# Kernel optimization log

Hardware: AMD Instinct MI355X
Metric: run time of the kernel (lower is better)

## Reference

```python
import jax, jax.numpy as jnp
import numpy as np

FD = 8  # flow_downsample


def equal_conv(x, w, b):
    # StyleGAN EqualConv2d: weight scaled by 1/sqrt(fan_in) at runtime, 3x3, pad 1
    scale = 1.0 / np.sqrt(w.shape[1] * w.shape[2] * w.shape[3])
    y = jax.lax.conv_general_dilated(
        x, w * scale, window_strides=(1, 1), padding=((1, 1), (1, 1)),
        dimension_numbers=('NCHW', 'OIHW', 'NCHW'))
    return y + b[None, :, None, None]


def identity_grid(Hf, Wf):
    # F.affine_grid(identity, align_corners=False): x fastest in last-dim slot 0
    xs = (jnp.arange(Wf, dtype=jnp.float32) + 0.5) * (2.0 / Wf) - 1.0
    ys = (jnp.arange(Hf, dtype=jnp.float32) + 0.5) * (2.0 / Hf) - 1.0
    gx, gy = jnp.meshgrid(xs, ys)  # (Hf, Wf)
    return jnp.stack([gx, gy], axis=-1)  # (Hf, Wf, 2)


def grid_sample_border(img, grid):
    # torch F.grid_sample(mode='bilinear', padding_mode='border', align_corners=False)
    N, C, H, W = img.shape
    x = (grid[..., 0] + 1.0) * (W * 0.5) - 0.5
    y = (grid[..., 1] + 1.0) * (H * 0.5) - 0.5
    x = jnp.clip(x, 0.0, W - 1.0)
    y = jnp.clip(y, 0.0, H - 1.0)
    x0 = jnp.floor(x); y0 = jnp.floor(y)
    wx = (x - x0).reshape(N, 1, -1)
    wy = (y - y0).reshape(N, 1, -1)
    x0i = x0.astype(jnp.int32); y0i = y0.astype(jnp.int32)
    x1i = jnp.minimum(x0i + 1, W - 1); y1i = jnp.minimum(y0i + 1, H - 1)
    imgf = img.reshape(N, C, H * W)
    def gather(yi, xi):
        idx = (yi * W + xi).reshape(N, 1, -1)
        return jnp.take_along_axis(imgf, idx, axis=2)  # (N, C, P)
    g00 = gather(y0i, x0i); g01 = gather(y0i, x1i)
    g10 = gather(y1i, x0i); g11 = gather(y1i, x1i)
    out = (g00 * (1 - wx) * (1 - wy) + g01 * wx * (1 - wy)
           + g10 * (1 - wx) * wy + g11 * wx * wy)
    return out.reshape(N, C, grid.shape[1], grid.shape[2])


def upsample_flow(flow_lr, mask):
    # flow_lr: (N,2,H,W), mask: (N, 9*FD*FD, H, W); RAFT convex upsampling
    N, _, H, W = flow_lr.shape
    mask = mask.reshape(N, 9, FD, FD, H, W)
    mask = jax.nn.softmax(mask, axis=1)
    padded = jnp.pad(FD * flow_lr, ((0, 0), (0, 0), (1, 1), (1, 1)))
    # F.unfold 3x3 pad 1, kernel positions row-major -> (N,2,9,H,W)
    patches = jnp.stack([padded[:, :, i:i + H, j:j + W]
                         for i in range(3) for j in range(3)], axis=2)
    up = jnp.einsum('nkuvhw,nckhw->ncuvhw', mask, patches)  # (N,2,FD,FD,H,W)
    up = up.transpose(0, 4, 2, 5, 3, 1)  # (N,H,FD,W,FD,2)
    return up.reshape(N, FD * H, FD * W, 2)


def setup_inputs() -> dict:
    key = jax.random.key(0)
    ks = jax.random.split(key, 9)
    N, C, H, W = 16, 256, 64, 64
    img = jax.random.normal(ks[0], (N, 3, FD * H, FD * W), dtype=jnp.float32)
    features = jax.random.normal(ks[1], (N, C, H, W), dtype=jnp.float32) * 0.5
    base_warp = (jnp.broadcast_to(jnp.eye(2, 3, dtype=jnp.float32), (N, 2, 3))
                 + 0.1 * jax.random.normal(ks[2], (N, 2, 3), dtype=jnp.float32))
    fan = 1.0  # raw weights are standard normal; EqualConv scales at runtime
    w_f1 = jax.random.normal(ks[3], (C, C, 3, 3), dtype=jnp.float32)
    b_f1 = jnp.zeros((C,), dtype=jnp.float32)
    w_f2 = jax.random.normal(ks[4], (2, C, 3, 3), dtype=jnp.float32) * 0.1
    b_f2 = jnp.zeros((2,), dtype=jnp.float32)
    w_m1 = jax.random.normal(ks[5], (C, C, 3, 3), dtype=jnp.float32)
    b_m1 = jnp.zeros((C,), dtype=jnp.float32)
    w_m2 = jax.random.normal(ks[6], (9 * FD * FD, C, 3, 3), dtype=jnp.float32)
    b_m2 = jnp.zeros((9 * FD * FD,), dtype=jnp.float32)
    return {"img": img, "features": features, "base_warp": base_warp,
            "w_f1": w_f1, "b_f1": b_f1, "w_f2": w_f2, "b_f2": b_f2,
            "w_m1": w_m1, "b_m1": b_m1, "w_m2": w_m2, "b_m2": b_m2}


def reference(img, features, base_warp, w_f1, b_f1, w_f2, b_f2,
              w_m1, b_m1, w_m2, b_m2):
    # compute_flow
    h = jax.nn.relu(equal_conv(features, w_f1, b_f1))
    flow_lr = equal_conv(h, w_f2, b_f2)                 # (N,2,H,W)
    hm = jax.nn.relu(equal_conv(features, w_m1, b_m1))
    mask = equal_conv(hm, w_m2, b_m2)                   # (N,576,H,W)
    delta_flow = upsample_flow(flow_lr, mask)           # (N,FD*H,FD*W,2)
    N, Hf, Wf, _ = delta_flow.shape
    flow = identity_grid(Hf, Wf)[None] + delta_flow
    # apply_affine(base_warp, flow)
    f = flow.reshape(N, -1, 2)
    f = jnp.concatenate([f, jnp.ones((N, f.shape[1], 1), dtype=f.dtype)], axis=2)
    flow = jnp.matmul(f, base_warp.transpose(0, 2, 1)).reshape(N, Hf, Wf, 2)
    out = grid_sample_border(img, flow)                 # (N,3,Hf,Wf)
    return (out, flow, delta_flow, flow)
```

## Files before the change

### kernel.cpp

```cpp
#include <hip/hip_runtime.h>
#include <cstdint>

typedef unsigned short u16;
typedef __bf16 bf8 __attribute__((ext_vector_type(8)));
typedef float f4 __attribute__((ext_vector_type(4)));
typedef u16 u16x4 __attribute__((ext_vector_type(4)));

#define NB 16
#define CH 256
#define HH 64
#define HP 66
#define KTOT 2304
#define SCALE (1.0f/48.0f)

#define OFF1 12582912
#define OFF2 20971520
#define OFF3 29360128

__device__ __forceinline__ unsigned bf16_rn(unsigned u) {
  return (u + 0x7fffu + ((u >> 16) & 1u)) >> 16;
}
__device__ __forceinline__ void split2(float x, u16 &h, u16 &l) {
  unsigned u = __float_as_uint(x);
  unsigned hb = bf16_rn(u);
  float hf = __uint_as_float(hb << 16);
  unsigned lb = bf16_rn(__float_as_uint(x - hf));
  h = (u16)hb; l = (u16)lb;
}

__device__ __forceinline__ void g2l16(const void* g, void* l) {
  __builtin_amdgcn_global_load_lds(
      (__attribute__((address_space(1))) void*)(uintptr_t)g,
      (__attribute__((address_space(3))) void*)(uint32_t)(uintptr_t)l,
      16, 0, 0);
}

__global__ void repack_feat(const float* __restrict__ f, u16* __restrict__ hi,
                            u16* __restrict__ lo) {
  __shared__ float t[64][65];
  int ny = blockIdx.x; int n = ny >> 6, y = ny & 63;
  int ci0 = blockIdx.y << 6;
  int tid = threadIdx.x;
  int a = tid >> 6, bl = tid & 63;
  const float* src = f + (((size_t)n*CH + ci0)*HH + y)*HH;
  #pragma unroll
  for (int i = 0; i < 16; i++) {
    int ci = i*4 + a;
    t[ci][bl] = src[(size_t)ci*4096 + bl];
  }
  __syncthreads();
  size_t base = (((size_t)n*HP + (y+1))*HP + 1)*CH + ci0;
  #pragma unroll
  for (int i = 0; i < 16; i++) {
    int x = i*4 + a;
    float v = t[bl][x];
    u16 hv, lv; split2(v, hv, lv);
    hi[base + (size_t)x*CH + bl] = hv;
    lo[base + (size_t)x*CH + bl] = lv;
  }
}

__global__ void repack_w(const float* __restrict__ w, u16* __restrict__ hi,
                         u16* __restrict__ lo, int Cout, int CoutPad) {
  int e = blockIdx.x*256 + threadIdx.x;
  if (e >= CoutPad*KTOT) return;
  int co = e / KTOT; int k = e - co*KTOT;
  int t = k >> 8, ci = k & 255;
  float v = 0.f;
  if (co < Cout) v = w[((size_t)co*CH + ci)*9 + t] * SCALE;
  u16 hv, lv; split2(v, hv, lv);
  hi[e] = hv; lo[e] = lv;
}

__global__ __launch_bounds__(256, 2) void conv_gemm(
    const u16* __restrict__ Ahi, const u16* __restrict__ Alo,
    const u16* __restrict__ Bhi, const u16* __restrict__ Blo,
    const float* __restrict__ bias,
    float* __restrict__ outF, u16* __restrict__ outHi, u16* __restrict__ outLo,
    int mode) {
  __shared__ u16 AsHi[8192], AsLo[8192], BsHi[8192], BsLo[8192];
  const int tid = threadIdx.x;
  const int wave = tid >> 6;
  const int lane = tid & 63;
  const int cb = blockIdx.x;
  const int mb = blockIdx.y;
  const int col0 = cb << 7;
  const int n = col0 >> 12;
  const int y0 = (col0 >> 6) & 63;

  const int l8 = lane & 7;
  const int r8 = lane >> 3;
  const int gsg = l8 ^ r8;

  int aBase[4], bBase[4], segOf[4];
  #pragma unroll
  for (int it = 0; it < 4; ++it) {
    int seg = wave*4 + it;
    segOf[it] = seg*512;
    int rl = seg*8 + r8;
    aBase[it] = (mb*128 + rl)*KTOT + gsg*8;
    int yy = y0 + (rl >> 6);
    int xx = rl & 63;
    bBase[it] = ((n*HP + yy)*HP + xx)*CH + gsg*8;
  }

  const f4 zero = {0.f, 0.f, 0.f, 0.f};
  f4 acc[4][4];
  #pragma unroll
  for (int i = 0; i < 4; i++)
    #pragma unroll
    for (int j = 0; j < 4; j++) acc[i][j] = zero;

  const int wm = (wave >> 1) << 6;
  const int wn = (wave & 1) << 6;
  const int r16 = lane & 15;
  const int kg = lane >> 4;
  const int sw = lane & 7;

  for (int kc = 0; kc < 36; ++kc) {
    int t = kc >> 2;
    int ci0 = (kc & 3) << 6;
    int dy = t / 3;
    int dx = t - dy*3;
    int bOff = (dy*HP + dx)*CH + ci0;
    int aOff = kc << 6;
    #pragma unroll
    for (int it = 0; it < 4; ++it) {
      g2l16(Ahi + aBase[it] + aOff, AsHi + segOf[it]);
      g2l16(Alo + aBase[it] + aOff, AsLo + segOf[it]);
      g2l16(Bhi + bBase[it] + bOff, BsHi + segOf[it]);
      g2l16(Blo + bBase[it] + bOff, BsLo + segOf[it]);
    }
    __syncthreads();
    #pragma unroll
    for (int ks = 0; ks < 2; ++ks) {
      int slot = ((ks << 2) + kg) ^ sw;
      bf8 ahi[4], alo[4], bhi[4], blo[4];
      #pragma unroll
      for (int mi = 0; mi < 4; ++mi) {
        int idx = (wm + mi*16 + r16)*64 + slot*8;
        ahi[mi] = *(const bf8*)(AsHi + idx);
        alo[mi] = *(const bf8*)(AsLo + idx);
      }
      #pragma unroll
      for (int ni = 0; ni < 4; ++ni) {
        int idx = (wn + ni*16 + r16)*64 + slot*8;
        bhi[ni] = *(const bf8*)(BsHi + idx);
        blo[ni] = *(const bf8*)(BsLo + idx);
      }
      #pragma unroll
      for (int mi = 0; mi < 4; ++mi)
        #pragma unroll
        for (int ni = 0; ni < 4; ++ni) {
          acc[mi][ni] = __builtin_amdgcn_mfma_f32_16x16x32_bf16(ahi[mi], bhi[ni], acc[mi][ni], 0, 0, 0);
          acc[mi][ni] = __builtin_amdgcn_mfma_f32_16x16x32_bf16(ahi[mi], blo[ni], acc[mi][ni], 0, 0, 0);
          acc[mi][ni] = __builtin_amdgcn_mfma_f32_16x16x32_bf16(alo[mi], bhi[ni], acc[mi][ni], 0, 0, 0);
        }
    }
    __syncthreads();
  }

  const int g4 = kg << 2;
  #pragma unroll
  for (int mi = 0; mi < 4; ++mi) {
    int coB = mb*128 + wm + mi*16 + g4;
    bool valid = (mode != 2) || (coB < 576);
    f4 bv = zero;
    if (valid) bv = *(const f4*)(bias + coB);
    #pragma unroll
    for (int ni = 0; ni < 4; ++ni) {
      int col = col0 + wn + ni*16 + r16;
      f4 v = acc[mi][ni];
      #pragma unroll
      for (int q = 0; q < 4; q++) v[q] += bv[q];
      if (mode == 2) {
        if (valid) *(f4*)(outF + (size_t)col*576 + coB) = v;
      } else {
        #pragma unroll
        for (int q = 0; q < 4; q++) v[q] = fmaxf(v[q], 0.f);
        int nn = col >> 12, yy = (col >> 6) & 63, xx = col & 63;
        size_t addr = (((size_t)nn*HP + yy + 1)*HP + xx + 1)*CH + coB;
        if (mode == 0) {
          *(f4*)(outF + addr) = v;
        } else {
          u16x4 hv, lv;
          #pragma unroll
          for (int q = 0; q < 4; q++) { u16 a_, b_; split2(v[q], a_, b_); hv[q] = a_; lv[q] = b_; }
          *(u16x4*)(outHi + addr) = hv;
          *(u16x4*)(outLo + addr) = lv;
        }
      }
    }
  }
}

__global__ __launch_bounds__(256) void conv_f2(const float* __restrict__ hpad,
    const float* __restrict__ w2, const float* __restrict__ b2,
    float* __restrict__ flow) {
  __shared__ float ws[2*KTOT];
  int tid = threadIdx.x;
  for (int i = tid; i < 2*KTOT; i += 256) {
    int c = i / KTOT; int r = i - c*KTOT;
    int t = r >> 8, ci = r & 255;
    ws[i] = w2[((size_t)c*CH + ci)*9 + t] * SCALE;
  }
  __syncthreads();
  int ny = blockIdx.x; int n = ny >> 6, y = ny & 63;
  int wv = tid >> 6, lane = tid & 63;
  for (int p = 0; p < 16; p++) {
    int x = wv*16 + p;
    float s0 = 0.f, s1 = 0.f;
    #pragma unroll
    for (int t = 0; t < 9; t++) {
      int dy = t / 3, dx = t - dy*3;
      const float* hb = hpad + (((size_t)n*HP + y + dy)*HP + x + dx)*CH;
      const float* wa = ws + t*256;
      const float* wb = ws + KTOT + t*256;
      #pragma unroll
      for (int j = 0; j < 4; j++) {
        int ci = j*64 + lane;
        float v = hb[ci];
        s0 = fmaf(v, wa[ci], s0);
        s1 = fmaf(v, wb[ci], s1);
      }
    }
    #pragma unroll
    for (int o = 32; o; o >>= 1) { s0 += __shfl_xor(s0, o); s1 += __shfl_xor(s1, o); }
    if (lane == 0) {
      size_t col = (size_t)n*4096 + y*64 + x;
      flow[col*2]   = s0 + b2[0];
      flow[col*2+1] = s1 + b2[1];
    }
  }
}

__global__ __launch_bounds__(256) void fuse_up(const float* __restrict__ mask,
    const float* __restrict__ flowlr, const float* __restrict__ img,
    const float* __restrict__ bwarp, float* __restrict__ out) {
  __shared__ float ms[4][576];
  __shared__ float fp[4][9][2];
  int tid = threadIdx.x;
  int cell = tid >> 6, lane = tid & 63;
  int b = blockIdx.x;
  int n = b >> 10;
  int h = (b >> 4) & 63;
  int w = ((b & 15) << 2) + cell;
  size_t col = (size_t)n*4096 + h*64 + w;
  #pragma unroll
  for (int r = 0; r < 9; r++) ms[cell][r*64 + lane] = mask[col*576 + r*64 + lane];
  if (lane < 18) {
    int k = lane >> 1, c = lane & 1;
    int hh = h + (k/3) - 1, ww = w + (k - (k/3)*3) - 1;
    float v = 0.f;
    if (hh >= 0 && hh < 64 && ww >= 0 && ww < 64)
      v = flowlr[(((size_t)n*4096) + hh*64 + ww)*2 + c];
    fp[cell][k][c] = 8.f * v;
  }
  __syncthreads();
  int u = lane >> 3, v = lane & 7;
  float mk[9]; float mx = -1e30f;
  #pragma unroll
  for (int k = 0; k < 9; k++) { mk[k] = ms[cell][k*64 + u*8 + v]; mx = fmaxf(mx, mk[k]); }
  float den = 0.f;
  #pragma unroll
  for (int k = 0; k < 9; k++) { mk[k] = __expf(mk[k] - mx); den += mk[k]; }
  float dxf = 0.f, dyf = 0.f;
  #pragma unroll
  for (int k = 0; k < 9; k++) { dxf += mk[k]*fp[cell][k][0]; dyf += mk[k]*fp[cell][k][1]; }
  dxf /= den; dyf /= den;
  int Y = h*8 + u, X = w*8 + v;
  float gx = (X + 0.5f)*(1.f/256.f) - 1.f;
  float gy = (Y + 0.5f)*(1.f/256.f) - 1.f;
  float fx = gx + dxf, fy = gy + dyf;
  const float* B = bwarp + n*6;
  float ax = B[0]*fx + B[1]*fy + B[2];
  float ay = B[3]*fx + B[4]*fy + B[5];
  size_t pix = (((size_t)n*512) + Y)*512 + X;
  *(float2*)(out + OFF1 + pix*2) = make_float2(ax, ay);
  *(float2*)(out + OFF2 + pix*2) = make_float2(dxf, dyf);
  *(float2*)(out + OFF3 + pix*2) = make_float2(ax, ay);
  float xs  = fminf(fmaxf((ax + 1.f)*256.f - 0.5f, 0.f), 511.f);
  float ysf = fminf(fmaxf((ay + 1.f)*256.f - 0.5f, 0.f), 511.f);
  float x0f = floorf(xs), y0f = floorf(ysf);
  int x0 = (int)x0f, y0 = (int)y0f;
  int x1 = min(x0 + 1, 511), y1 = min(y0 + 1, 511);
  float wx = xs - x0f, wy = ysf - y0f;
  #pragma unroll
  for (int c = 0; c < 3; c++) {
    const float* ip = img + ((size_t)(n*3 + c) << 18);
    float g00 = ip[y0*512 + x0], g01 = ip[y0*512 + x1];
    float g10 = ip[y1*512 + x0], g11 = ip[y1*512 + x1];
    float r = g00*(1.f-wx)*(1.f-wy) + g01*wx*(1.f-wy)
            + g10*(1.f-wx)*wy + g11*wx*wy;
    out[(((size_t)(n*3 + c))*512 + Y)*512 + X] = r;
  }
}

extern "C" void kernel_launch(void* const* d_in, const int* in_sizes, int n_in,
                              void* d_out, int out_size, void* d_ws, size_t ws_size,
                              hipStream_t stream) {
  const float* img   = (const float*)d_in[0];
  const float* feat  = (const float*)d_in[1];
  const float* bwarp = (const float*)d_in[2];
  const float* w_f1  = (const float*)d_in[3];
  const float* b_f1  = (const float*)d_in[4];
  const float* w_f2  = (const float*)d_in[5];
  const float* b_f2  = (const float*)d_in[6];
  const float* w_m1  = (const float*)d_in[7];
  const float* b_m1  = (const float*)d_in[8];
  const float* w_m2  = (const float*)d_in[9];
  const float* b_m2  = (const float*)d_in[10];
  float* out = (float*)d_out;

  char* ws = (char*)d_ws;
  size_t off = 0;
  auto alloc = [&](size_t bytes) -> char* {
    char* p = ws + off; off += (bytes + 255) & ~(size_t)255; return p;
  };
  const size_t NPAD = (size_t)NB*HP*HP*CH;
  u16* feat_hi = (u16*)alloc(NPAD*2);
  u16* feat_lo = (u16*)alloc(NPAD*2);
  float* h_pad = (float*)alloc(NPAD*4);
  u16* hm_hi   = (u16*)alloc(NPAD*2);
  u16* hm_lo   = (u16*)alloc(NPAD*2);
  u16* A1_hi   = (u16*)alloc((size_t)256*KTOT*2);
  u16* A1_lo   = (u16*)alloc((size_t)256*KTOT*2);
  u16* Am1_hi  = (u16*)alloc((size_t)256*KTOT*2);
  u16* Am1_lo  = (u16*)alloc((size_t)256*KTOT*2);
  u16* Am2_hi  = (u16*)alloc((size_t)640*KTOT*2);
  u16* Am2_lo  = (u16*)alloc((size_t)640*KTOT*2);
  float* mask  = (float*)alloc((size_t)65536*576*4);
  float* flowlr= (float*)alloc((size_t)65536*2*4);
  (void)ws_size; (void)in_sizes; (void)n_in; (void)out_size;

  hipMemsetAsync(feat_hi, 0, NPAD*2, stream);
  hipMemsetAsync(feat_lo, 0, NPAD*2, stream);
  hipMemsetAsync(h_pad,  0, NPAD*4, stream);
  hipMemsetAsync(hm_hi,  0, NPAD*2, stream);
  hipMemsetAsync(hm_lo,  0, NPAD*2, stream);

  repack_feat<<<dim3(1024, 4), 256, 0, stream>>>(feat, feat_hi, feat_lo);
  repack_w<<<(256*KTOT + 255)/256, 256, 0, stream>>>(w_f1, A1_hi,  A1_lo,  256, 256);
  repack_w<<<(256*KTOT + 255)/256, 256, 0, stream>>>(w_m1, Am1_hi, Am1_lo, 256, 256);
  repack_w<<<(640*KTOT + 255)/256, 256, 0, stream>>>(w_m2, Am2_hi, Am2_lo, 576, 640);

  conv_gemm<<<dim3(512, 2), 256, 0, stream>>>(A1_hi,  A1_lo,  feat_hi, feat_lo, b_f1,
                                              h_pad, nullptr, nullptr, 0);
  conv_gemm<<<dim3(512, 2), 256, 0, stream>>>(Am1_hi, Am1_lo, feat_hi, feat_lo, b_m1,
                                              nullptr, hm_hi, hm_lo, 1);
  conv_gemm<<<dim3(512, 5), 256, 0, stream>>>(Am2_hi, Am2_lo, hm_hi, hm_lo, b_m2,
                                              mask, nullptr, nullptr, 2);
  conv_f2<<<1024, 256, 0, stream>>>(h_pad, w_f2, b_f2, flowlr);
  fuse_up<<<16384, 256, 0, stream>>>(mask, flowlr, img, bwarp, out);
}
```

Baseline: 1.316 ms.

## Zero only padded halos and remap GEMM blocks for XCD-local B reuse

Five full-buffer memsets are replaced with one small kernel that zeroes only the one-pixel halo border of each padded activation buffer, because the interiors are overwritten later. The conv GEMM grid is flattened and remapped so that consecutive block IDs, which the hardware spreads round-robin across the 8 XCDs, give each XCD a contiguous range of column blocks with all M-blocks of a column block together. This should improve L2 reuse of the B (activation) tiles. The change relies on the interior of each buffer being fully written before it is read, which holds for h_pad and hm only if the conv epilogues write every interior element.

```diff
diff --git a/kernel.cpp b/kernel.cpp
--- a/kernel.cpp
+++ b/kernel.cpp
@@ -33,6 +33,26 @@
       (__attribute__((address_space(1))) void*)(uintptr_t)g,
       (__attribute__((address_space(3))) void*)(uint32_t)(uintptr_t)l,
       16, 0, 0);
+}
+
+__global__ void zero_halo(u16* __restrict__ b0, u16* __restrict__ b1,
+                          u16* __restrict__ b2, u16* __restrict__ b3,
+                          float* __restrict__ f0) {
+  int seg = blockIdx.x;
+  int n = seg / 260, r = seg - n*260;
+  int y, x;
+  if (r < 66)       { y = 0;       x = r; }
+  else if (r < 132) { y = 65;      x = r - 66; }
+  else if (r < 196) { y = r - 131; x = 0; }
+  else              { y = r - 195; x = 65; }
+  size_t base = (((size_t)n*HP + y)*HP + x)*CH + threadIdx.x*4;
+  const u16x4 z16 = {0,0,0,0};
+  const f4 z32 = {0.f,0.f,0.f,0.f};
+  *(u16x4*)(b0 + base) = z16;
+  *(u16x4*)(b1 + base) = z16;
+  *(u16x4*)(b2 + base) = z16;
+  *(u16x4*)(b3 + base) = z16;
+  *(f4*)(f0 + base) = z32;
 }
 
 __global__ void repack_feat(const float* __restrict__ f, u16* __restrict__ hi,
@@ -77,13 +97,16 @@
     const u16* __restrict__ Bhi, const u16* __restrict__ Blo,
     const float* __restrict__ bias,
     float* __restrict__ outF, u16* __restrict__ outHi, u16* __restrict__ outLo,
-    int mode) {
+    int mode, int MB) {
   __shared__ u16 AsHi[8192], AsLo[8192], BsHi[8192], BsLo[8192];
   const int tid = threadIdx.x;
   const int wave = tid >> 6;
   const int lane = tid & 63;
-  const int cb = blockIdx.x;
-  const int mb = blockIdx.y;
+  int gidx = blockIdx.x;
+  int xcd = gidx & 7, s = gidx >> 3;
+  int cbl = s / MB;
+  int mb = s - cbl*MB;
+  int cb = xcd*64 + cbl;
   const int col0 = cb << 7;
   const int n = col0 >> 12;
   const int y0 = (col0 >> 6) & 63;
@@ -333,23 +356,19 @@
   float* flowlr= (float*)alloc((size_t)65536*2*4);
   (void)ws_size; (void)in_sizes; (void)n_in; (void)out_size;
 
-  hipMemsetAsync(feat_hi, 0, NPAD*2, stream);
-  hipMemsetAsync(feat_lo, 0, NPAD*2, stream);
-  hipMemsetAsync(h_pad,  0, NPAD*4, stream);
-  hipMemsetAsync(hm_hi,  0, NPAD*2, stream);
-  hipMemsetAsync(hm_lo,  0, NPAD*2, stream);
+  zero_halo<<<NB*260, 64, 0, stream>>>(feat_hi, feat_lo, hm_hi, hm_lo, h_pad);
 
   repack_feat<<<dim3(1024, 4), 256, 0, stream>>>(feat, feat_hi, feat_lo);
   repack_w<<<(256*KTOT + 255)/256, 256, 0, stream>>>(w_f1, A1_hi,  A1_lo,  256, 256);
   repack_w<<<(256*KTOT + 255)/256, 256, 0, stream>>>(w_m1, Am1_hi, Am1_lo, 256, 256);
   repack_w<<<(640*KTOT + 255)/256, 256, 0, stream>>>(w_m2, Am2_hi, Am2_lo, 576, 640);
 
-  conv_gemm<<<dim3(512, 2), 256, 0, stream>>>(A1_hi,  A1_lo,  feat_hi, feat_lo, b_f1,
-                                              h_pad, nullptr, nullptr, 0);
-  conv_gemm<<<dim3(512, 2), 256, 0, stream>>>(Am1_hi, Am1_lo, feat_hi, feat_lo, b_m1,
-                                              nullptr, hm_hi, hm_lo, 1);
-  conv_gemm<<<dim3(512, 5), 256, 0, stream>>>(Am2_hi, Am2_lo, hm_hi, hm_lo, b_m2,
-                                              mask, nullptr, nullptr, 2);
+  conv_gemm<<<1024, 256, 0, stream>>>(A1_hi,  A1_lo,  feat_hi, feat_lo, b_f1,
+                                      h_pad, nullptr, nullptr, 0, 2);
+  conv_gemm<<<1024, 256, 0, stream>>>(Am1_hi, Am1_lo, feat_hi, feat_lo, b_m1,
+                                      nullptr, hm_hi, hm_lo, 1, 2);
+  conv_gemm<<<2560, 256, 0, stream>>>(Am2_hi, Am2_lo, hm_hi, hm_lo, b_m2,
+                                      mask, nullptr, nullptr, 2, 5);
   conv_f2<<<1024, 256, 0, stream>>>(h_pad, w_f2, b_f2, flowlr);
   fuse_up<<<16384, 256, 0, stream>>>(mask, flowlr, img, bwarp, out);
 }
```

After: 1.232 ms. 6.4% less time.
